# Optimization experiments

Measured on AMD Instinct MI355X. Metric: run time of the kernel, lower is better.

The kernel has to match this reference:

```python
import jax, jax.numpy as jnp
import numpy as np

B = 2048
NUM_FEATURES = 40960
M = 256
N = 32
K = 32
MAX_EVAL = 10000.0  # Chess_Lib.MAX_EVAL stand-in
SPARSITY = 32.0 / NUM_FEATURES  # ~32 active HalfKP features per position


def _xavier(key, shape):
    fan_out, fan_in = shape
    limit = np.sqrt(6.0 / (fan_in + fan_out)).astype(np.float32)
    return jax.random.uniform(key, shape, jnp.float32, -limit, limit)


def setup_inputs() -> dict:
    key = jax.random.key(0)
    ks = jax.random.split(key, 8)
    # ~32-hot sparse binary feature vectors (HalfKP style)
    wf = (jax.random.uniform(ks[0], (B, NUM_FEATURES)) < SPARSITY).astype(jnp.float32)
    bf = (jax.random.uniform(ks[1], (B, NUM_FEATURES)) < SPARSITY).astype(jnp.float32)
    stm = jnp.round(jax.random.uniform(ks[2], (B, 1))).astype(jnp.float32)
    return {
        "white_features": wf,
        "black_features": bf,
        "stm": stm,
        "ft_w": _xavier(ks[3], (M, NUM_FEATURES)),
        "ft_b": jnp.zeros((M,), jnp.float32),
        "l1_w": _xavier(ks[4], (N, 2 * M)),
        "l1_b": jnp.zeros((N,), jnp.float32),
        "l2_w": _xavier(ks[5], (K, N)),
        "l2_b": jnp.zeros((K,), jnp.float32),
        "l3_w": _xavier(ks[6], (1, K)),
        "l3_b": jnp.zeros((1,), jnp.float32),
    }


def reference(white_features, black_features, stm, ft_w, ft_b,
              l1_w, l1_b, l2_w, l2_b, l3_w, l3_b):
    # feature transformer: [B,F] @ [F,M] -> [B,M]
    w = white_features @ ft_w.T + ft_b
    b = black_features @ ft_w.T + ft_b
    acc = stm * jnp.concatenate([w, b], axis=1) + (1.0 - stm) * jnp.concatenate([b, w], axis=1)
    l1_x = jnp.clip(acc, 0.0, 1.0)
    l2_x = jnp.clip(l1_x @ l1_w.T + l1_b, 0.0, 1.0)
    l3_x = jnp.clip(l2_x @ l2_w.T + l2_b, 0.0, 1.0)
    ev = jnp.clip(l3_x @ l3_w.T + l3_b, 0.0, 1.0)
    # align_eval without the python int() cast (kept batched/differentiable)
    return (ev - 0.5) * 2.0 * MAX_EVAL
```

## Files before the change

kernel.cpp:

```cpp
#include <hip/hip_runtime.h>
#include <hip/hip_bf16.h>
#include <hip/hip_cooperative_groups.h>

namespace cg = cooperative_groups;

#define NF 40960
#define MD 256
#define BATCH 2048
#define CAP 512
#define NTILE ((NF / 64) * (MD / 64))

typedef float vf4 __attribute__((ext_vector_type(4)));

__device__ __forceinline__ float clip01(float v) {
    return fminf(fmaxf(v, 0.0f), 1.0f);
}

struct ScanSmem {
    int idxW[CAP], idxB[CAP];
    int nW, nB;
    float xsh[512];
    float red[32][9];
    float ysh[32], zsh[32];
};
union Smem {
    float tile[64][65];
    ScanSmem s;
};

__device__ __forceinline__ void scan_pos(ScanSmem& s, int t, int pos,
    const float* __restrict__ wf, const float* __restrict__ bfeat)
{
    if (t == 0) { s.nW = 0; s.nB = 0; }
    __syncthreads();
    const vf4* wf4 = (const vf4*)(wf + (size_t)pos * NF);
    const vf4* bf4 = (const vf4*)(bfeat + (size_t)pos * NF);
    #pragma unroll 4
    for (int i = t; i < NF / 4; i += 256) {
        vf4 v = __builtin_nontemporal_load(wf4 + i);
        if (v.x + v.y + v.z + v.w != 0.0f) {
            if (v.x != 0.0f) { int p = atomicAdd(&s.nW, 1); if (p < CAP) s.idxW[p] = 4 * i;     }
            if (v.y != 0.0f) { int p = atomicAdd(&s.nW, 1); if (p < CAP) s.idxW[p] = 4 * i + 1; }
            if (v.z != 0.0f) { int p = atomicAdd(&s.nW, 1); if (p < CAP) s.idxW[p] = 4 * i + 2; }
            if (v.w != 0.0f) { int p = atomicAdd(&s.nW, 1); if (p < CAP) s.idxW[p] = 4 * i + 3; }
        }
        vf4 u = __builtin_nontemporal_load(bf4 + i);
        if (u.x + u.y + u.z + u.w != 0.0f) {
            if (u.x != 0.0f) { int p = atomicAdd(&s.nB, 1); if (p < CAP) s.idxB[p] = 4 * i;     }
            if (u.y != 0.0f) { int p = atomicAdd(&s.nB, 1); if (p < CAP) s.idxB[p] = 4 * i + 1; }
            if (u.z != 0.0f) { int p = atomicAdd(&s.nB, 1); if (p < CAP) s.idxB[p] = 4 * i + 2; }
            if (u.w != 0.0f) { int p = atomicAdd(&s.nB, 1); if (p < CAP) s.idxB[p] = 4 * i + 3; }
        }
    }
    __syncthreads();
}

__device__ __forceinline__ void gather_tail(ScanSmem& s, int t, int pos,
    const float* __restrict__ gt, int transposed,
    const float* __restrict__ ft_b, const float* __restrict__ stm,
    const float* __restrict__ l1_w, const float* __restrict__ l1_b,
    const float* __restrict__ l2_w, const float* __restrict__ l2_b,
    const float* __restrict__ l3_w, const float* __restrict__ l3_b,
    float* __restrict__ out)
{
    const int cw = min(s.nW, CAP);
    const int cb = min(s.nB, CAP);

    float accW = ft_b[t];
    float accB = ft_b[t];
    if (transposed) {
        for (int j = 0; j < cw; ++j) accW += gt[(size_t)s.idxW[j] * MD + t];
        for (int j = 0; j < cb; ++j) accB += gt[(size_t)s.idxB[j] * MD + t];
    } else {
        const float* row = gt + (size_t)t * NF;
        for (int j = 0; j < cw; ++j) accW += row[s.idxW[j]];
        for (int j = 0; j < cb; ++j) accB += row[s.idxB[j]];
    }

    const float sv = stm[pos];
    s.xsh[t]       = clip01(sv * accW + (1.0f - sv) * accB);
    s.xsh[256 + t] = clip01(sv * accB + (1.0f - sv) * accW);
    __syncthreads();

    {
        const int n = t & 31;
        const int c = t >> 5;
        const float* w1 = l1_w + (size_t)n * 512 + c * 64;
        const float* xx = s.xsh + c * 64;
        float p = 0.0f;
        #pragma unroll
        for (int j = 0; j < 64; ++j) p += xx[j] * w1[j];
        s.red[n][c] = p;
    }
    __syncthreads();
    if (t < 32) {
        float v = l1_b[t];
        #pragma unroll
        for (int c = 0; c < 8; ++c) v += s.red[t][c];
        s.ysh[t] = clip01(v);
    }
    __syncthreads();
    if (t < 32) {
        float v = l2_b[t];
        const float* w2 = l2_w + t * 32;
        #pragma unroll
        for (int j = 0; j < 32; ++j) v += s.ysh[j] * w2[j];
        s.zsh[t] = clip01(v);
    }
    __syncthreads();
    if (t == 0) {
        float v = l3_b[0];
        #pragma unroll
        for (int j = 0; j < 32; ++j) v += s.zsh[j] * l3_w[j];
        out[pos] = (clip01(v) - 0.5f) * 20000.0f;
    }
}

__global__ __launch_bounds__(256, 8) void nnue_coop(
    const float* __restrict__ wf, const float* __restrict__ bfeat,
    const float* __restrict__ stm, const float* __restrict__ ft_w,
    const float* __restrict__ ft_b,
    const float* __restrict__ l1_w, const float* __restrict__ l1_b,
    const float* __restrict__ l2_w, const float* __restrict__ l2_b,
    const float* __restrict__ l3_w, const float* __restrict__ l3_b,
    float* __restrict__ out, float* __restrict__ ftT)
{
    __shared__ Smem u;
    const int b = blockIdx.x;
    const int t = threadIdx.x;

    for (int tl = b; tl < NTILE; tl += BATCH) {
        const int f0 = (tl % (NF / 64)) * 64;
        const int m0 = (tl / (NF / 64)) * 64;
        const int tx = t & 63;
        const int ty = t >> 6;
        #pragma unroll
        for (int r = ty; r < 64; r += 4)
            u.tile[r][tx] = ft_w[(size_t)(m0 + r) * NF + f0 + tx];
        __syncthreads();
        #pragma unroll
        for (int r = ty; r < 64; r += 4)
            ftT[(size_t)(f0 + r) * MD + m0 + tx] = u.tile[tx][r];
        __syncthreads();
    }

    scan_pos(u.s, t, b, wf, bfeat);

    __threadfence();
    cg::this_grid().sync();
    __threadfence();

    gather_tail(u.s, t, b, ftT, 1, ft_b, stm,
                l1_w, l1_b, l2_w, l2_b, l3_w, l3_b, out);
}

__global__ __launch_bounds__(256) void transpose_ft(const float* __restrict__ in,
                                                    float* __restrict__ outT) {
    __shared__ float tile[64][65];
    const int b = blockIdx.x;
    const int f0 = (b % (NF / 64)) * 64;
    const int m0 = (b / (NF / 64)) * 64;
    const int tx = threadIdx.x & 63;
    const int ty = threadIdx.x >> 6;
    #pragma unroll
    for (int r = ty; r < 64; r += 4)
        tile[r][tx] = in[(size_t)(m0 + r) * NF + f0 + tx];
    __syncthreads();
    #pragma unroll
    for (int r = ty; r < 64; r += 4)
        outT[(size_t)(f0 + r) * MD + m0 + tx] = tile[tx][r];
}

__global__ __launch_bounds__(256) void nnue_plain(
    const float* __restrict__ wf, const float* __restrict__ bfeat,
    const float* __restrict__ stm, const float* __restrict__ gt,
    const float* __restrict__ ft_b,
    const float* __restrict__ l1_w, const float* __restrict__ l1_b,
    const float* __restrict__ l2_w, const float* __restrict__ l2_b,
    const float* __restrict__ l3_w, const float* __restrict__ l3_b,
    float* __restrict__ out, int transposed)
{
    __shared__ Smem u;
    const int pos = blockIdx.x;
    const int t = threadIdx.x;
    scan_pos(u.s, t, pos, wf, bfeat);
    gather_tail(u.s, t, pos, gt, transposed, ft_b, stm,
                l1_w, l1_b, l2_w, l2_b, l3_w, l3_b, out);
}

extern "C" void kernel_launch(void* const* d_in, const int* in_sizes, int n_in,
                              void* d_out, int out_size, void* d_ws, size_t ws_size,
                              hipStream_t stream) {
    const float* wf    = (const float*)d_in[0];
    const float* bfeat = (const float*)d_in[1];
    const float* stm   = (const float*)d_in[2];
    const float* ft_w  = (const float*)d_in[3];
    const float* ft_b  = (const float*)d_in[4];
    const float* l1_w  = (const float*)d_in[5];
    const float* l1_b  = (const float*)d_in[6];
    const float* l2_w  = (const float*)d_in[7];
    const float* l2_b  = (const float*)d_in[8];
    const float* l3_w  = (const float*)d_in[9];
    const float* l3_b  = (const float*)d_in[10];
    float* out = (float*)d_out;

    float* ftT = (float*)d_ws;
    const size_t needT = (size_t)NF * MD * sizeof(float);
    const bool haveWs = ws_size >= needT;

    if (haveWs) {
        int dev = 0, coopOK = 0, numCU = 0, maxBlk = 0;
        hipGetDevice(&dev);
        hipDeviceGetAttribute(&coopOK, hipDeviceAttributeCooperativeLaunch, dev);
        hipDeviceGetAttribute(&numCU, hipDeviceAttributeMultiprocessorCount, dev);
        hipOccupancyMaxActiveBlocksPerMultiprocessor(&maxBlk, nnue_coop, 256, 0);
        if (coopOK && (long)maxBlk * numCU >= BATCH) {
            void* args[] = {
                (void*)&wf, (void*)&bfeat, (void*)&stm, (void*)&ft_w, (void*)&ft_b,
                (void*)&l1_w, (void*)&l1_b, (void*)&l2_w, (void*)&l2_b,
                (void*)&l3_w, (void*)&l3_b, (void*)&out, (void*)&ftT };
            hipError_t e = hipLaunchCooperativeKernel(
                (const void*)nnue_coop, dim3(BATCH), dim3(256), args, 0, stream);
            if (e == hipSuccess) return;
        }
    }

    if (haveWs) {
        transpose_ft<<<NTILE, 256, 0, stream>>>(ft_w, ftT);
        nnue_plain<<<BATCH, 256, 0, stream>>>(
            wf, bfeat, stm, ftT, ft_b,
            l1_w, l1_b, l2_w, l2_b, l3_w, l3_b, out, 1);
    } else {
        nnue_plain<<<BATCH, 256, 0, stream>>>(
            wf, bfeat, stm, ft_w, ft_b,
            l1_w, l1_b, l2_w, l2_b, l3_w, l3_b, out, 0);
    }
}
```

Measured before the change: 692.6 us.

## Process two positions per block with batched scans and padded gathers

Replaces the cooperative kernel with one launching 1024 blocks, each handling two positions. The feature scan issues 16 outstanding nontemporal vector loads per iteration across four feature rows to raise memory-level parallelism. The index lists are padded to a multiple of four with a sentinel that points to a zeroed extra row of the transposed weights, so the gather loop can issue 16 independent loads per step. This needs one extra workspace row and halves the number of resident blocks, so per-block latency hiding now depends on the deeper load batching.

```diff
diff --git a/kernel.cpp b/kernel.cpp
--- a/kernel.cpp
+++ b/kernel.cpp
@@ -7,6 +7,7 @@
 #define NF 40960
 #define MD 256
 #define BATCH 2048
+#define NBLK 1024
 #define CAP 512
 #define NTILE ((NF / 64) * (MD / 64))
 
@@ -14,6 +15,162 @@
 
 __device__ __forceinline__ float clip01(float v) {
     return fminf(fmaxf(v, 0.0f), 1.0f);
+}
+
+struct Scan2 {
+    int idx[4][CAP];
+    int n[4];
+    float xsh[512];
+    float red[32][9];
+    float ysh[32], zsh[32];
+};
+union Smem2 {
+    float tile[64][65];
+    Scan2 s;
+};
+
+__device__ __forceinline__ void mlp_tail2(Scan2& s, int t, int pos,
+    float accW, float accB,
+    const float* __restrict__ stm,
+    const float* __restrict__ l1_w, const float* __restrict__ l1_b,
+    const float* __restrict__ l2_w, const float* __restrict__ l2_b,
+    const float* __restrict__ l3_w, const float* __restrict__ l3_b,
+    float* __restrict__ out)
+{
+    const float sv = stm[pos];
+    s.xsh[t]       = clip01(sv * accW + (1.0f - sv) * accB);
+    s.xsh[256 + t] = clip01(sv * accB + (1.0f - sv) * accW);
+    __syncthreads();
+    {
+        const int n = t & 31;
+        const int c = t >> 5;
+        const float* w1 = l1_w + (size_t)n * 512 + c * 64;
+        const float* xx = s.xsh + c * 64;
+        float p = 0.0f;
+        #pragma unroll
+        for (int j = 0; j < 64; ++j) p += xx[j] * w1[j];
+        s.red[n][c] = p;
+    }
+    __syncthreads();
+    if (t < 32) {
+        float v = l1_b[t];
+        #pragma unroll
+        for (int c = 0; c < 8; ++c) v += s.red[t][c];
+        s.ysh[t] = clip01(v);
+    }
+    __syncthreads();
+    if (t < 32) {
+        float v = l2_b[t];
+        const float* w2 = l2_w + t * 32;
+        #pragma unroll
+        for (int j = 0; j < 32; ++j) v += s.ysh[j] * w2[j];
+        s.zsh[t] = clip01(v);
+    }
+    __syncthreads();
+    if (t == 0) {
+        float v = l3_b[0];
+        #pragma unroll
+        for (int j = 0; j < 32; ++j) v += s.zsh[j] * l3_w[j];
+        out[pos] = (clip01(v) - 0.5f) * 20000.0f;
+    }
+    __syncthreads();
+}
+
+__global__ __launch_bounds__(256, 4) void nnue_coop2(
+    const float* __restrict__ wf, const float* __restrict__ bfeat,
+    const float* __restrict__ stm, const float* __restrict__ ft_w,
+    const float* __restrict__ ft_b,
+    const float* __restrict__ l1_w, const float* __restrict__ l1_b,
+    const float* __restrict__ l2_w, const float* __restrict__ l2_b,
+    const float* __restrict__ l3_w, const float* __restrict__ l3_b,
+    float* __restrict__ out, float* __restrict__ ftT)
+{
+    __shared__ Smem2 u;
+    const int b = blockIdx.x;
+    const int t = threadIdx.x;
+
+    for (int tl = b; tl < NTILE; tl += NBLK) {
+        const int f0 = (tl % (NF / 64)) * 64;
+        const int m0 = (tl / (NF / 64)) * 64;
+        const int tx = t & 63;
+        const int ty = t >> 6;
+        #pragma unroll
+        for (int r = ty; r < 64; r += 4)
+            u.tile[r][tx] = ft_w[(size_t)(m0 + r) * NF + f0 + tx];
+        __syncthreads();
+        #pragma unroll
+        for (int r = ty; r < 64; r += 4)
+            ftT[(size_t)(f0 + r) * MD + m0 + tx] = u.tile[tx][r];
+        __syncthreads();
+    }
+    if (b == 0) ftT[(size_t)NF * MD + t] = 0.0f;
+
+    const int p0 = b;
+    const int p1 = b + NBLK;
+    if (t < 4) u.s.n[t] = 0;
+    __syncthreads();
+    {
+        const vf4* sp[4] = {
+            (const vf4*)(wf    + (size_t)p0 * NF),
+            (const vf4*)(bfeat + (size_t)p0 * NF),
+            (const vf4*)(wf    + (size_t)p1 * NF),
+            (const vf4*)(bfeat + (size_t)p1 * NF) };
+        for (int k = 0; k < 10; ++k) {
+            vf4 r[16];
+            #pragma unroll
+            for (int l = 0; l < 4; ++l)
+                #pragma unroll
+                for (int q = 0; q < 4; ++q)
+                    r[l * 4 + q] = __builtin_nontemporal_load(
+                        sp[l] + (t + (k * 4 + q) * 256));
+            #pragma unroll
+            for (int l = 0; l < 4; ++l)
+                #pragma unroll
+                for (int q = 0; q < 4; ++q) {
+                    vf4 v = r[l * 4 + q];
+                    if (__builtin_expect(v.x + v.y + v.z + v.w != 0.0f, 0)) {
+                        const int fb = (t + (k * 4 + q) * 256) * 4;
+                        if (v.x != 0.0f) { int p = atomicAdd(&u.s.n[l], 1); if (p < CAP) u.s.idx[l][p] = fb;     }
+                        if (v.y != 0.0f) { int p = atomicAdd(&u.s.n[l], 1); if (p < CAP) u.s.idx[l][p] = fb + 1; }
+                        if (v.z != 0.0f) { int p = atomicAdd(&u.s.n[l], 1); if (p < CAP) u.s.idx[l][p] = fb + 2; }
+                        if (v.w != 0.0f) { int p = atomicAdd(&u.s.n[l], 1); if (p < CAP) u.s.idx[l][p] = fb + 3; }
+                    }
+                }
+        }
+    }
+    __syncthreads();
+
+    const int c0 = min(u.s.n[0], CAP), c1 = min(u.s.n[1], CAP);
+    const int c2 = min(u.s.n[2], CAP), c3 = min(u.s.n[3], CAP);
+    const int m = (max(max(c0, c1), max(c2, c3)) + 3) & ~3;
+    if (t < 4) {
+        const int cl = min(u.s.n[t], CAP);
+        for (int k2 = cl; k2 < m; ++k2) u.s.idx[t][k2] = NF;
+    }
+
+    __threadfence();
+    cg::this_grid().sync();
+    __threadfence();
+
+    const float bias = ft_b[t];
+    float a0 = 0.0f, a1 = 0.0f, a2 = 0.0f, a3 = 0.0f;
+    for (int j = 0; j < m; j += 4) {
+        float v[16];
+        #pragma unroll
+        for (int l = 0; l < 4; ++l)
+            #pragma unroll
+            for (int q = 0; q < 4; ++q)
+                v[l * 4 + q] = ftT[(size_t)u.s.idx[l][j + q] * MD + t];
+        a0 += (v[0]  + v[1])  + (v[2]  + v[3]);
+        a1 += (v[4]  + v[5])  + (v[6]  + v[7]);
+        a2 += (v[8]  + v[9])  + (v[10] + v[11]);
+        a3 += (v[12] + v[13]) + (v[14] + v[15]);
+    }
+
+    mlp_tail2(u.s, t, p0, bias + a0, bias + a1, stm,
+              l1_w, l1_b, l2_w, l2_b, l3_w, l3_b, out);
+    mlp_tail2(u.s, t, p1, bias + a2, bias + a3, stm,
+              l1_w, l1_b, l2_w, l2_b, l3_w, l3_b, out);
 }
 
 struct ScanSmem {
@@ -44,12 +201,12 @@
             if (v.z != 0.0f) { int p = atomicAdd(&s.nW, 1); if (p < CAP) s.idxW[p] = 4 * i + 2; }
             if (v.w != 0.0f) { int p = atomicAdd(&s.nW, 1); if (p < CAP) s.idxW[p] = 4 * i + 3; }
         }
-        vf4 u = __builtin_nontemporal_load(bf4 + i);
-        if (u.x + u.y + u.z + u.w != 0.0f) {
-            if (u.x != 0.0f) { int p = atomicAdd(&s.nB, 1); if (p < CAP) s.idxB[p] = 4 * i;     }
-            if (u.y != 0.0f) { int p = atomicAdd(&s.nB, 1); if (p < CAP) s.idxB[p] = 4 * i + 1; }
-            if (u.z != 0.0f) { int p = atomicAdd(&s.nB, 1); if (p < CAP) s.idxB[p] = 4 * i + 2; }
-            if (u.w != 0.0f) { int p = atomicAdd(&s.nB, 1); if (p < CAP) s.idxB[p] = 4 * i + 3; }
+        vf4 uu = __builtin_nontemporal_load(bf4 + i);
+        if (uu.x + uu.y + uu.z + uu.w != 0.0f) {
+            if (uu.x != 0.0f) { int p = atomicAdd(&s.nB, 1); if (p < CAP) s.idxB[p] = 4 * i;     }
+            if (uu.y != 0.0f) { int p = atomicAdd(&s.nB, 1); if (p < CAP) s.idxB[p] = 4 * i + 1; }
+            if (uu.z != 0.0f) { int p = atomicAdd(&s.nB, 1); if (p < CAP) s.idxB[p] = 4 * i + 2; }
+            if (uu.w != 0.0f) { int p = atomicAdd(&s.nB, 1); if (p < CAP) s.idxB[p] = 4 * i + 3; }
         }
     }
     __syncthreads();
@@ -114,44 +271,6 @@
         for (int j = 0; j < 32; ++j) v += s.zsh[j] * l3_w[j];
         out[pos] = (clip01(v) - 0.5f) * 20000.0f;
     }
-}
-
-__global__ __launch_bounds__(256, 8) void nnue_coop(
-    const float* __restrict__ wf, const float* __restrict__ bfeat,
-    const float* __restrict__ stm, const float* __restrict__ ft_w,
-    const float* __restrict__ ft_b,
-    const float* __restrict__ l1_w, const float* __restrict__ l1_b,
-    const float* __restrict__ l2_w, const float* __restrict__ l2_b,
-    const float* __restrict__ l3_w, const float* __restrict__ l3_b,
-    float* __restrict__ out, float* __restrict__ ftT)
-{
-    __shared__ Smem u;
-    const int b = blockIdx.x;
-    const int t = threadIdx.x;
-
-    for (int tl = b; tl < NTILE; tl += BATCH) {
-        const int f0 = (tl % (NF / 64)) * 64;
-        const int m0 = (tl / (NF / 64)) * 64;
-        const int tx = t & 63;
-        const int ty = t >> 6;
-        #pragma unroll
-        for (int r = ty; r < 64; r += 4)
-            u.tile[r][tx] = ft_w[(size_t)(m0 + r) * NF + f0 + tx];
-        __syncthreads();
-        #pragma unroll
-        for (int r = ty; r < 64; r += 4)
-            ftT[(size_t)(f0 + r) * MD + m0 + tx] = u.tile[tx][r];
-        __syncthreads();
-    }
-
-    scan_pos(u.s, t, b, wf, bfeat);
-
-    __threadfence();
-    cg::this_grid().sync();
-    __threadfence();
-
-    gather_tail(u.s, t, b, ftT, 1, ft_b, stm,
-                l1_w, l1_b, l2_w, l2_b, l3_w, l3_b, out);
 }
 
 __global__ __launch_bounds__(256) void transpose_ft(const float* __restrict__ in,
@@ -205,27 +324,27 @@
     float* out = (float*)d_out;
 
     float* ftT = (float*)d_ws;
-    const size_t needT = (size_t)NF * MD * sizeof(float);
-    const bool haveWs = ws_size >= needT;
-
-    if (haveWs) {
+    const size_t needCoop = (size_t)(NF + 1) * MD * sizeof(float);
+    const size_t needT    = (size_t)NF * MD * sizeof(float);
+
+    if (ws_size >= needCoop) {
         int dev = 0, coopOK = 0, numCU = 0, maxBlk = 0;
         hipGetDevice(&dev);
         hipDeviceGetAttribute(&coopOK, hipDeviceAttributeCooperativeLaunch, dev);
         hipDeviceGetAttribute(&numCU, hipDeviceAttributeMultiprocessorCount, dev);
-        hipOccupancyMaxActiveBlocksPerMultiprocessor(&maxBlk, nnue_coop, 256, 0);
-        if (coopOK && (long)maxBlk * numCU >= BATCH) {
+        hipOccupancyMaxActiveBlocksPerMultiprocessor(&maxBlk, nnue_coop2, 256, 0);
+        if (coopOK && (long)maxBlk * numCU >= NBLK) {
             void* args[] = {
                 (void*)&wf, (void*)&bfeat, (void*)&stm, (void*)&ft_w, (void*)&ft_b,
                 (void*)&l1_w, (void*)&l1_b, (void*)&l2_w, (void*)&l2_b,
                 (void*)&l3_w, (void*)&l3_b, (void*)&out, (void*)&ftT };
             hipError_t e = hipLaunchCooperativeKernel(
-                (const void*)nnue_coop, dim3(BATCH), dim3(256), args, 0, stream);
+                (const void*)nnue_coop2, dim3(NBLK), dim3(256), args, 0, stream);
             if (e == hipSuccess) return;
         }
     }
 
-    if (haveWs) {
+    if (ws_size >= needT) {
         transpose_ft<<<NTILE, 256, 0, stream>>>(ft_w, ftT);
         nnue_plain<<<BATCH, 256, 0, stream>>>(
             wf, bfeat, stm, ftT, ft_b,
```

Result: no change. 690.0 us (-0.4%).
